# Kernel optimization log

Hardware: AMD Instinct MI355X
Metric: run time of the kernel (lower is better)

Reference implementation:

```python
import jax, jax.numpy as jnp
import numpy as np

C = 1024
H = 64
W = 64


def _conv1x1(x, Wt, b):
    # x: [1, Cin, H, W], Wt: [Cout, Cin] -> [1, Cout, H, W]
    return jnp.einsum('oc,bchw->bohw', Wt, x) + b[None, :, None, None]


def setup_inputs() -> dict:
    key = jax.random.key(0)
    ks = jax.random.split(key, 12)
    sc = 1.0 / np.sqrt(C)
    return {
        'x_f': jax.random.normal(ks[0], (1, C, H, W), jnp.float32),
        'x_m': jax.random.normal(ks[1], (1, C, H, W), jnp.float32),
        'x_l': jax.random.normal(ks[2], (1, C, H, W), jnp.float32),
        'Wq': jax.random.normal(ks[3], (C // 2, C), jnp.float32) * sc,
        'bq': jax.random.normal(ks[4], (C // 2,), jnp.float32) * sc,
        'Wk1': jax.random.normal(ks[5], (C // 2, C), jnp.float32) * sc,
        'bk1': jax.random.normal(ks[6], (C // 2,), jnp.float32) * sc,
        'Wk2': jax.random.normal(ks[7], (C // 2, C), jnp.float32) * sc,
        'bk2': jax.random.normal(ks[8], (C // 2,), jnp.float32) * sc,
        'Wv': jax.random.normal(ks[9], (C, C), jnp.float32) * sc,
        'bv': jax.random.normal(ks[10], (C,), jnp.float32) * sc,
        'gamma': jax.random.normal(ks[11], (1,), jnp.float32),
    }


def reference(x_f, x_m, x_l, Wq, bq, Wk1, bk1, Wk2, bk2, Wv, bv, gamma):
    c = x_f.shape[1]
    h, w = x_f.shape[2], x_f.shape[3]
    # torch .view(1, C, -1) on a [1, C/2, H, W] tensor: row-major reshape to [C, H*W/2]
    q = _conv1x1(x_m, Wq, bq).reshape(c, -1).T      # [HW/2, C]
    kf = _conv1x1(x_f, Wk1, bk1).reshape(c, -1)     # [C, HW/2]
    kl = _conv1x1(x_l, Wk2, bk2).reshape(c, -1)     # [C, HW/2]
    att_f = jax.nn.softmax(kf @ q, axis=-1)         # [C, C]
    att_l = jax.nn.softmax(kl @ q, axis=-1)         # [C, C]
    v = _conv1x1(x_m, Wv, bv).reshape(c, -1)        # [C, HW]
    out = att_f @ v + att_l @ v                     # [C, HW]
    out = out.reshape(1, c, h, w)
    return gamma * out + (x_l + x_f) / 2
```

## Files before the change

kernel.cpp:

```cpp
#include <hip/hip_runtime.h>
#include <math.h>


typedef __attribute__((ext_vector_type(8))) short    bf16x8;
typedef __attribute__((ext_vector_type(4))) float    f32x4;

__device__ __forceinline__ unsigned short f2bf(float x) {
    unsigned u = __float_as_uint(x);
    u += 0x7FFFu + ((u >> 16) & 1u);
    return (unsigned short)(u >> 16);
}
__device__ __forceinline__ float bf2f(unsigned short h) {
    return __uint_as_float(((unsigned)h) << 16);
}
__device__ __forceinline__ void split2(float x, unsigned short& h, unsigned short& l) {
    h = f2bf(x);
    l = f2bf(x - bf2f(h));
}

__device__ __forceinline__ void gld16(const unsigned short* g, unsigned short* l) {
    __builtin_amdgcn_global_load_lds(
        (const __attribute__((address_space(1))) unsigned int*)g,
        (__attribute__((address_space(3))) unsigned int*)l,
        16, 0, 0);
}

__global__ __launch_bounds__(256) void weights_split_k(
    const float* __restrict__ Wq, const float* __restrict__ Wk1,
    const float* __restrict__ Wk2, const float* __restrict__ Wv,
    unsigned short* __restrict__ Wqh, unsigned short* __restrict__ Wql,
    unsigned short* __restrict__ Wk1h, unsigned short* __restrict__ Wk1l,
    unsigned short* __restrict__ Wk2h, unsigned short* __restrict__ Wk2l,
    unsigned short* __restrict__ Wvh, unsigned short* __restrict__ Wvl)
{
    const int gi = blockIdx.x;
    const float* src; unsigned short *H, *L; int base;
    if (gi < 512)       { src = Wq;  H = Wqh;  L = Wql;  base = gi; }
    else if (gi < 1024) { src = Wk1; H = Wk1h; L = Wk1l; base = gi - 512; }
    else if (gi < 1536) { src = Wk2; H = Wk2h; L = Wk2l; base = gi - 1024; }
    else                { src = Wv;  H = Wvh;  L = Wvl;  base = gi - 1536; }
    const size_t i = (size_t)base * 1024 + threadIdx.x * 4;
    const float4 v = *(const float4*)(src + i);
    ushort4 h, l;
    split2(v.x, h.x, l.x); split2(v.y, h.y, l.y);
    split2(v.z, h.z, l.z); split2(v.w, h.w, l.w);
    *(ushort4*)(H + i) = h;
    *(ushort4*)(L + i) = l;
}

__global__ __launch_bounds__(256) void transpose3_k(
    const float* __restrict__ x0, const float* __restrict__ x1,
    const float* __restrict__ x2,
    unsigned short* __restrict__ t0h, unsigned short* __restrict__ t0l,
    unsigned short* __restrict__ t1h, unsigned short* __restrict__ t1l,
    unsigned short* __restrict__ t2h, unsigned short* __restrict__ t2l)
{
    const float* X; unsigned short *Th, *Tl;
    if (blockIdx.z == 0)      { X = x0; Th = t0h; Tl = t0l; }
    else if (blockIdx.z == 1) { X = x1; Th = t1h; Tl = t1l; }
    else                      { X = x2; Th = t2h; Tl = t2l; }

    __shared__ float t[32 * 33];
    const int tid = threadIdx.x;
    const int c0 = blockIdx.y * 32;
    const int p0 = blockIdx.x * 32;

    const int cl = tid >> 3;
    const int p4 = (tid & 7) * 4;
    const float4 v = *(const float4*)(X + (size_t)(c0 + cl) * 4096 + p0 + p4);
    t[(p4 + 0) * 33 + cl] = v.x;
    t[(p4 + 1) * 33 + cl] = v.y;
    t[(p4 + 2) * 33 + cl] = v.z;
    t[(p4 + 3) * 33 + cl] = v.w;
    __syncthreads();

    const int pl = tid >> 3;
    const int c4 = (tid & 7) * 4;
    ushort4 h, l;
    split2(t[pl * 33 + c4 + 0], h.x, l.x);
    split2(t[pl * 33 + c4 + 1], h.y, l.y);
    split2(t[pl * 33 + c4 + 2], h.z, l.z);
    split2(t[pl * 33 + c4 + 3], h.w, l.w);
    const size_t o = (size_t)(p0 + pl) * 1024 + c0 + c4;
    *(ushort4*)(Th + o) = h;
    *(ushort4*)(Tl + o) = l;
}

__global__ __launch_bounds__(256) void transpose1_k(
    const float* __restrict__ X,
    unsigned short* __restrict__ Th, unsigned short* __restrict__ Tl)
{
    __shared__ float t[32 * 33];
    const int tid = threadIdx.x;
    const int c0 = blockIdx.y * 32;
    const int p0 = blockIdx.x * 32;

    const int cl = tid >> 3;
    const int p4 = (tid & 7) * 4;
    const float4 v = *(const float4*)(X + (size_t)(c0 + cl) * 4096 + p0 + p4);
    t[(p4 + 0) * 33 + cl] = v.x;
    t[(p4 + 1) * 33 + cl] = v.y;
    t[(p4 + 2) * 33 + cl] = v.z;
    t[(p4 + 3) * 33 + cl] = v.w;
    __syncthreads();

    const int pl = tid >> 3;
    const int c4 = (tid & 7) * 4;
    ushort4 h, l;
    split2(t[pl * 33 + c4 + 0], h.x, l.x);
    split2(t[pl * 33 + c4 + 1], h.y, l.y);
    split2(t[pl * 33 + c4 + 2], h.z, l.z);
    split2(t[pl * 33 + c4 + 3], h.w, l.w);
    const size_t o = (size_t)(p0 + pl) * 1024 + c0 + c4;
    *(ushort4*)(Th + o) = h;
    *(ushort4*)(Tl + o) = l;
}

__device__ __forceinline__ void gemm_core(
    const unsigned short* __restrict__ Ah, const unsigned short* __restrict__ Al,
    const unsigned short* __restrict__ Bh, const unsigned short* __restrict__ Bl,
    int ldk, int kbeg, int kend, int m0, int n0,
    unsigned short* As_h, unsigned short* As_l,
    unsigned short* Bs_h, unsigned short* Bs_l,
    f32x4 (&acc)[4][4])
{
    const int tid  = threadIdx.x;
    const int lane = tid & 63;
    const int wv   = tid >> 6;
    const int wm   = (wv >> 1) * 64;
    const int wn   = (wv & 1) * 64;
    const int lr   = lane & 15;
    const int quad = lane >> 4;

    const unsigned short* gsrc = (wv == 0) ? Ah : (wv == 1) ? Al : (wv == 2) ? Bh : Bl;
    unsigned short* ldst = (wv == 0) ? As_h : (wv == 1) ? As_l : (wv == 2) ? Bs_h : Bs_l;
    const int tile0 = (wv < 2) ? m0 : n0;
    const int lrow = lane >> 2;
    const int gseg = ((lane & 3) - ((lane >> 3) & 3)) & 3;
    const unsigned short* gp[8];
#pragma unroll
    for (int t = 0; t < 8; ++t)
        gp[t] = gsrc + (size_t)(tile0 + t * 16 + lrow) * ldk + kbeg + gseg * 8;

    const int rdseg = (quad + (lr >> 1)) & 3;

    for (int k0 = kbeg; k0 < kend; k0 += 32) {
        __syncthreads();
#pragma unroll
        for (int t = 0; t < 8; ++t) {
            gld16(gp[t], ldst + t * 512);
            gp[t] += 32;
        }
        __syncthreads();

        bf16x8 afh[4], afl[4], bfh[4], bfl[4];
#pragma unroll
        for (int i = 0; i < 4; ++i) {
            const int ra = (wm + i * 16 + lr) * 32 + rdseg * 8;
            afh[i] = *(const bf16x8*)(As_h + ra);
            afl[i] = *(const bf16x8*)(As_l + ra);
            const int rb = (wn + i * 16 + lr) * 32 + rdseg * 8;
            bfh[i] = *(const bf16x8*)(Bs_h + rb);
            bfl[i] = *(const bf16x8*)(Bs_l + rb);
        }
#pragma unroll
        for (int i = 0; i < 4; ++i)
#pragma unroll
            for (int j = 0; j < 4; ++j) {
                acc[i][j] = __builtin_amdgcn_mfma_f32_16x16x32_bf16(afh[i], bfh[j], acc[i][j], 0, 0, 0);
                acc[i][j] = __builtin_amdgcn_mfma_f32_16x16x32_bf16(afh[i], bfl[j], acc[i][j], 0, 0, 0);
                acc[i][j] = __builtin_amdgcn_mfma_f32_16x16x32_bf16(afl[i], bfh[j], acc[i][j], 0, 0, 0);
            }
    }
}

#define GEMM_PROLOGUE()                                                 \
    __shared__ __align__(16) unsigned short As_h[128 * 32];             \
    __shared__ __align__(16) unsigned short As_l[128 * 32];             \
    __shared__ __align__(16) unsigned short Bs_h[128 * 32];             \
    __shared__ __align__(16) unsigned short Bs_l[128 * 32];             \
    f32x4 acc[4][4];                                                    \
    _Pragma("unroll") for (int i = 0; i < 4; ++i)                       \
    _Pragma("unroll") for (int j = 0; j < 4; ++j)                       \
    _Pragma("unroll") for (int r = 0; r < 4; ++r) acc[i][j][r] = 0.f;   \
    const int lane = threadIdx.x & 63;                                  \
    const int wv   = threadIdx.x >> 6;                                  \
    const int wm   = (wv >> 1) * 64;                                    \
    const int wn   = (wv & 1) * 64;                                     \
    const int lr   = lane & 15;                                         \
    const int quad = lane >> 4;                                         \
    (void)lane; (void)wv;

__global__ __launch_bounds__(256) void conv_all_k(
    const unsigned short* __restrict__ Wqh, const unsigned short* __restrict__ Wql,
    const unsigned short* __restrict__ Wk1h, const unsigned short* __restrict__ Wk1l,
    const unsigned short* __restrict__ Wk2h, const unsigned short* __restrict__ Wk2l,
    const unsigned short* __restrict__ Wvh, const unsigned short* __restrict__ Wvl,
    const unsigned short* __restrict__ xmTh, const unsigned short* __restrict__ xmTl,
    const unsigned short* __restrict__ xfTh, const unsigned short* __restrict__ xfTl,
    const unsigned short* __restrict__ xlTh, const unsigned short* __restrict__ xlTl,
    const float* __restrict__ bq, const float* __restrict__ bk1,
    const float* __restrict__ bk2, const float* __restrict__ bv,
    unsigned short* __restrict__ Qh, unsigned short* __restrict__ Ql,
    unsigned short* __restrict__ Kfh, unsigned short* __restrict__ Kfl,
    unsigned short* __restrict__ Klh, unsigned short* __restrict__ Kll,
    float* __restrict__ V)
{
    GEMM_PROLOGUE();
    const int mt = blockIdx.y;
    const unsigned short *Ah, *Al, *Bh, *Bl;
    const float* bias;
    unsigned short *Ch = nullptr, *Cl = nullptr;
    float* Cv = nullptr;
    int mloc;
    if (mt < 4) {
        Ah = Wqh;  Al = Wql;  Bh = xmTh; Bl = xmTl; bias = bq;
        Ch = Qh;   Cl = Ql;   mloc = mt * 128;
    } else if (mt < 8) {
        Ah = Wk1h; Al = Wk1l; Bh = xfTh; Bl = xfTl; bias = bk1;
        Ch = Kfh;  Cl = Kfl;  mloc = (mt - 4) * 128;
    } else if (mt < 12) {
        Ah = Wk2h; Al = Wk2l; Bh = xlTh; Bl = xlTl; bias = bk2;
        Ch = Klh;  Cl = Kll;  mloc = (mt - 8) * 128;
    } else {
        Ah = Wvh;  Al = Wvl;  Bh = xmTh; Bl = xmTl; bias = bv;
        Cv = V;    mloc = (mt - 12) * 128;
    }
    const int n0 = blockIdx.x * 128;

    gemm_core(Ah, Al, Bh, Bl, 1024, 0, 1024, mloc, n0, As_h, As_l, Bs_h, Bs_l, acc);

#pragma unroll
    for (int i = 0; i < 4; ++i) {
        const int mb = mloc + wm + i * 16 + quad * 4;
#pragma unroll
        for (int j = 0; j < 4; ++j) {
            const int nn = n0 + wn + j * 16 + lr;
#pragma unroll
            for (int r = 0; r < 4; ++r) {
                const float v = acc[i][j][r] + bias[mb + r];
                const size_t idx = (size_t)(mb + r) * 4096 + nn;
                if (Cv) {
                    Cv[idx] = v;
                } else {
                    unsigned short h, l;
                    split2(v, h, l);
                    Ch[idx] = h;
                    Cl[idx] = l;
                }
            }
        }
    }
}

__global__ __launch_bounds__(256) void logits_fused_k(
    const unsigned short* __restrict__ Kfh, const unsigned short* __restrict__ Kfl,
    const unsigned short* __restrict__ Klh, const unsigned short* __restrict__ Kll,
    const unsigned short* __restrict__ Qh, const unsigned short* __restrict__ Ql,
    float* __restrict__ Sfp, float* __restrict__ Slp)
{
    GEMM_PROLOGUE();
    const int which = blockIdx.z >> 2;
    const int slice = blockIdx.z & 3;
    const unsigned short* Ah = which ? Klh : Kfh;
    const unsigned short* Al = which ? Kll : Kfl;
    float* out = (which ? Slp : Sfp) + (size_t)slice * 1024 * 1024;
    const int m0 = blockIdx.y * 128;
    const int n0 = blockIdx.x * 128;

    gemm_core(Ah, Al, Qh, Ql, 2048, slice * 512, slice * 512 + 512, m0, n0,
              As_h, As_l, Bs_h, Bs_l, acc);

#pragma unroll
    for (int i = 0; i < 4; ++i) {
        const int mb = m0 + wm + i * 16 + quad * 4;
#pragma unroll
        for (int j = 0; j < 4; ++j) {
            const int nn = n0 + wn + j * 16 + lr;
#pragma unroll
            for (int r = 0; r < 4; ++r)
                out[(size_t)(mb + r) * 1024 + nn] = acc[i][j][r];
        }
    }
}

__global__ __launch_bounds__(256) void gemm_final_k(
    const unsigned short* __restrict__ Amh, const unsigned short* __restrict__ Aml,
    const unsigned short* __restrict__ VTh, const unsigned short* __restrict__ VTl,
    float* __restrict__ out,
    const float* __restrict__ xf, const float* __restrict__ xl,
    const float* __restrict__ gamma)
{
    GEMM_PROLOGUE();
    const int m0 = blockIdx.y * 128;
    const int n0 = blockIdx.x * 128;

    gemm_core(Amh, Aml, VTh, VTl, 1024, 0, 1024, m0, n0,
              As_h, As_l, Bs_h, Bs_l, acc);

    const float g = gamma[0];
#pragma unroll
    for (int i = 0; i < 4; ++i) {
        const int mb = m0 + wm + i * 16 + quad * 4;
#pragma unroll
        for (int j = 0; j < 4; ++j) {
            const int nn = n0 + wn + j * 16 + lr;
#pragma unroll
            for (int r = 0; r < 4; ++r) {
                const size_t idx = (size_t)(mb + r) * 4096 + nn;
                out[idx] = g * acc[i][j][r] + 0.5f * (xf[idx] + xl[idx]);
            }
        }
    }
}

__global__ __launch_bounds__(256) void softmax_add4_k(
    const float* __restrict__ Sfp, const float* __restrict__ Slp,
    unsigned short* __restrict__ Ah, unsigned short* __restrict__ Al)
{
    const int row = blockIdx.x;
    const int tid = threadIdx.x;
    __shared__ float red[8];
    const size_t base = (size_t)row * 1024 + tid * 4;
    const size_t SL = (size_t)1024 * 1024;

    float4 vf = *(const float4*)(Sfp + base);
    float4 vl = *(const float4*)(Slp + base);
#pragma unroll
    for (int s = 1; s < 4; ++s) {
        const float4 a = *(const float4*)(Sfp + s * SL + base);
        const float4 b = *(const float4*)(Slp + s * SL + base);
        vf.x += a.x; vf.y += a.y; vf.z += a.z; vf.w += a.w;
        vl.x += b.x; vl.y += b.y; vl.z += b.z; vl.w += b.w;
    }

    float mf = fmaxf(fmaxf(vf.x, vf.y), fmaxf(vf.z, vf.w));
    float ml = fmaxf(fmaxf(vl.x, vl.y), fmaxf(vl.z, vl.w));
#pragma unroll
    for (int off = 32; off; off >>= 1) {
        mf = fmaxf(mf, __shfl_down(mf, off, 64));
        ml = fmaxf(ml, __shfl_down(ml, off, 64));
    }
    const int wave = tid >> 6;
    if ((tid & 63) == 0) { red[wave] = mf; red[4 + wave] = ml; }
    __syncthreads();
    mf = fmaxf(fmaxf(red[0], red[1]), fmaxf(red[2], red[3]));
    ml = fmaxf(fmaxf(red[4], red[5]), fmaxf(red[6], red[7]));
    __syncthreads();

    const float4 ef = make_float4(expf(vf.x - mf), expf(vf.y - mf),
                                  expf(vf.z - mf), expf(vf.w - mf));
    const float4 el = make_float4(expf(vl.x - ml), expf(vl.y - ml),
                                  expf(vl.z - ml), expf(vl.w - ml));
    float sf = ef.x + ef.y + ef.z + ef.w;
    float sl = el.x + el.y + el.z + el.w;
#pragma unroll
    for (int off = 32; off; off >>= 1) {
        sf += __shfl_down(sf, off, 64);
        sl += __shfl_down(sl, off, 64);
    }
    if ((tid & 63) == 0) { red[wave] = sf; red[4 + wave] = sl; }
    __syncthreads();
    sf = red[0] + red[1] + red[2] + red[3];
    sl = red[4] + red[5] + red[6] + red[7];

    const float rf = 1.f / sf, rl = 1.f / sl;
    ushort4 h, l;
    split2(ef.x * rf + el.x * rl, h.x, l.x);
    split2(ef.y * rf + el.y * rl, h.y, l.y);
    split2(ef.z * rf + el.z * rl, h.z, l.z);
    split2(ef.w * rf + el.w * rl, h.w, l.w);
    *(ushort4*)(Ah + base) = h;
    *(ushort4*)(Al + base) = l;
}

__global__ void noop_k(float* p) { if (threadIdx.x == 1024) p[0] = 0.f; }

extern "C" void kernel_launch(void* const* d_in, const int* in_sizes, int n_in,
                              void* d_out, int out_size, void* d_ws, size_t ws_size,
                              hipStream_t stream) {
    (void)in_sizes; (void)n_in; (void)out_size;
    const float* xf  = (const float*)d_in[0];
    const float* xm  = (const float*)d_in[1];
    const float* xl  = (const float*)d_in[2];
    const float* Wq  = (const float*)d_in[3];
    const float* bq  = (const float*)d_in[4];
    const float* Wk1 = (const float*)d_in[5];
    const float* bk1 = (const float*)d_in[6];
    const float* Wk2 = (const float*)d_in[7];
    const float* bk2 = (const float*)d_in[8];
    const float* Wv  = (const float*)d_in[9];
    const float* bv  = (const float*)d_in[10];
    const float* gamma = (const float*)d_in[11];
    float* out = (float*)d_out;

    const size_t MB = 1024 * 1024;
    if (ws_size < 98 * MB) {
        noop_k<<<dim3(1), dim3(64), 0, stream>>>((float*)d_ws);
        return;
    }

    char* p = (char*)d_ws;
    unsigned short* xmT_h = (unsigned short*)(p + 0 * MB);
    unsigned short* xmT_l = (unsigned short*)(p + 8 * MB);
    unsigned short* xfT_h = (unsigned short*)(p + 16 * MB);
    unsigned short* xfT_l = (unsigned short*)(p + 24 * MB);
    unsigned short* xlT_h = (unsigned short*)(p + 32 * MB);
    unsigned short* xlT_l = (unsigned short*)(p + 40 * MB);
    unsigned short* Wq_h  = (unsigned short*)(p + 48 * MB);
    unsigned short* Wq_l  = (unsigned short*)(p + 49 * MB);
    unsigned short* Wk1_h = (unsigned short*)(p + 50 * MB);
    unsigned short* Wk1_l = (unsigned short*)(p + 51 * MB);
    unsigned short* Wk2_h = (unsigned short*)(p + 52 * MB);
    unsigned short* Wk2_l = (unsigned short*)(p + 53 * MB);
    unsigned short* Wv_h  = (unsigned short*)(p + 54 * MB);
    unsigned short* Wv_l  = (unsigned short*)(p + 56 * MB);
    unsigned short* Q_h   = (unsigned short*)(p + 58 * MB);
    unsigned short* Q_l   = (unsigned short*)(p + 62 * MB);
    unsigned short* Kf_h  = (unsigned short*)(p + 66 * MB);
    unsigned short* Kf_l  = (unsigned short*)(p + 70 * MB);
    unsigned short* Kl_h  = (unsigned short*)(p + 74 * MB);
    unsigned short* Kl_l  = (unsigned short*)(p + 78 * MB);
    float*          V     = (float*)(p + 82 * MB);
    float*          Sfp  = (float*)(p + 16 * MB);
    float*          Slp  = (float*)(p + 32 * MB);
    unsigned short* VT_h = xmT_h;
    unsigned short* VT_l = xmT_l;
    unsigned short* Am_h = (unsigned short*)(p + 74 * MB);
    unsigned short* Am_l = (unsigned short*)(p + 76 * MB);

    const dim3 blk(256);
    transpose3_k<<<dim3(128, 32, 3), blk, 0, stream>>>(
        xm, xf, xl, xmT_h, xmT_l, xfT_h, xfT_l, xlT_h, xlT_l);
    weights_split_k<<<dim3(2560), blk, 0, stream>>>(
        Wq, Wk1, Wk2, Wv, Wq_h, Wq_l, Wk1_h, Wk1_l, Wk2_h, Wk2_l, Wv_h, Wv_l);
    conv_all_k<<<dim3(32, 20), blk, 0, stream>>>(
        Wq_h, Wq_l, Wk1_h, Wk1_l, Wk2_h, Wk2_l, Wv_h, Wv_l,
        xmT_h, xmT_l, xfT_h, xfT_l, xlT_h, xlT_l,
        bq, bk1, bk2, bv,
        Q_h, Q_l, Kf_h, Kf_l, Kl_h, Kl_l, V);
    logits_fused_k<<<dim3(8, 8, 8), blk, 0, stream>>>(
        Kf_h, Kf_l, Kl_h, Kl_l, Q_h, Q_l, Sfp, Slp);
    transpose1_k<<<dim3(128, 32), blk, 0, stream>>>(V, VT_h, VT_l);
    softmax_add4_k<<<dim3(1024), blk, 0, stream>>>(Sfp, Slp, Am_h, Am_l);
    gemm_final_k<<<dim3(32, 8), blk, 0, stream>>>(
        Am_h, Am_l, VT_h, VT_l, out, xf, xl, gamma);
}
```

Before: 303.6 us.

## Double-buffer B tiles in LDS, load A directly to registers, drop third term in final GEMM

The shared GEMM core now keeps only the B operand in LDS, double-buffered so the next k-slice load is issued before the current slice is computed, which removes one barrier per iteration. The A operand fragments are read straight from global memory into registers instead of being staged through LDS. A template parameter lets the final attention-times-V GEMM skip the lo(A)*hi(B) MFMA term, cutting its MFMA count by a third. Skipping that term lowers the precision of the final GEMM, and the direct global A loads may add latency and uncoalesced traffic.

```diff
diff --git a/kernel.cpp b/kernel.cpp
--- a/kernel.cpp
+++ b/kernel.cpp
@@ -116,11 +116,11 @@
     *(ushort4*)(Tl + o) = l;
 }
 
+template<int TERMS>
 __device__ __forceinline__ void gemm_core(
     const unsigned short* __restrict__ Ah, const unsigned short* __restrict__ Al,
     const unsigned short* __restrict__ Bh, const unsigned short* __restrict__ Bl,
     int ldk, int kbeg, int kend, int m0, int n0,
-    unsigned short* As_h, unsigned short* As_l,
     unsigned short* Bs_h, unsigned short* Bs_l,
     f32x4 (&acc)[4][4])
 {
@@ -132,36 +132,56 @@
     const int lr   = lane & 15;
     const int quad = lane >> 4;
 
-    const unsigned short* gsrc = (wv == 0) ? Ah : (wv == 1) ? Al : (wv == 2) ? Bh : Bl;
-    unsigned short* ldst = (wv == 0) ? As_h : (wv == 1) ? As_l : (wv == 2) ? Bs_h : Bs_l;
-    const int tile0 = (wv < 2) ? m0 : n0;
+    const unsigned short* gsrc = (wv < 2) ? Bh : Bl;
+    unsigned short* ldst = (wv < 2) ? Bs_h : Bs_l;
+    const int tt0  = (wv & 1) * 4;
     const int lrow = lane >> 2;
     const int gseg = ((lane & 3) - ((lane >> 3) & 3)) & 3;
-    const unsigned short* gp[8];
-#pragma unroll
-    for (int t = 0; t < 8; ++t)
-        gp[t] = gsrc + (size_t)(tile0 + t * 16 + lrow) * ldk + kbeg + gseg * 8;
+    const unsigned short* gp[4];
+#pragma unroll
+    for (int u = 0; u < 4; ++u)
+        gp[u] = gsrc + (size_t)(n0 + (tt0 + u) * 16 + lrow) * ldk + kbeg + gseg * 8;
+
+    const unsigned short* ap[4];
+    const unsigned short* apl[4];
+#pragma unroll
+    for (int i = 0; i < 4; ++i) {
+        const size_t ro = (size_t)(m0 + wm + i * 16 + lr) * ldk + kbeg + quad * 8;
+        ap[i] = Ah + ro;
+        apl[i] = (TERMS == 3) ? (Al + ro) : nullptr;
+    }
 
     const int rdseg = (quad + (lr >> 1)) & 3;
 
+#pragma unroll
+    for (int u = 0; u < 4; ++u) {
+        gld16(gp[u], ldst + (tt0 + u) * 512);
+        gp[u] += 32;
+    }
+
+    int buf = 0;
     for (int k0 = kbeg; k0 < kend; k0 += 32) {
         __syncthreads();
-#pragma unroll
-        for (int t = 0; t < 8; ++t) {
-            gld16(gp[t], ldst + t * 512);
-            gp[t] += 32;
-        }
-        __syncthreads();
-
-        bf16x8 afh[4], afl[4], bfh[4], bfl[4];
+
+        bf16x8 afh[4], afl[4];
 #pragma unroll
         for (int i = 0; i < 4; ++i) {
-            const int ra = (wm + i * 16 + lr) * 32 + rdseg * 8;
-            afh[i] = *(const bf16x8*)(As_h + ra);
-            afl[i] = *(const bf16x8*)(As_l + ra);
-            const int rb = (wn + i * 16 + lr) * 32 + rdseg * 8;
-            bfh[i] = *(const bf16x8*)(Bs_h + rb);
-            bfl[i] = *(const bf16x8*)(Bs_l + rb);
+            afh[i] = *(const bf16x8*)ap[i];  ap[i] += 32;
+            if (TERMS == 3) { afl[i] = *(const bf16x8*)apl[i]; apl[i] += 32; }
+        }
+        if (k0 + 32 < kend) {
+#pragma unroll
+            for (int u = 0; u < 4; ++u) {
+                gld16(gp[u], ldst + (buf ^ 1) * 4096 + (tt0 + u) * 512);
+                gp[u] += 32;
+            }
+        }
+        bf16x8 bfh[4], bfl[4];
+#pragma unroll
+        for (int j = 0; j < 4; ++j) {
+            const int rb = buf * 4096 + (wn + j * 16 + lr) * 32 + rdseg * 8;
+            bfh[j] = *(const bf16x8*)(Bs_h + rb);
+            bfl[j] = *(const bf16x8*)(Bs_l + rb);
         }
 #pragma unroll
         for (int i = 0; i < 4; ++i)
@@ -169,16 +189,16 @@
             for (int j = 0; j < 4; ++j) {
                 acc[i][j] = __builtin_amdgcn_mfma_f32_16x16x32_bf16(afh[i], bfh[j], acc[i][j], 0, 0, 0);
                 acc[i][j] = __builtin_amdgcn_mfma_f32_16x16x32_bf16(afh[i], bfl[j], acc[i][j], 0, 0, 0);
-                acc[i][j] = __builtin_amdgcn_mfma_f32_16x16x32_bf16(afl[i], bfh[j], acc[i][j], 0, 0, 0);
+                if (TERMS == 3)
+                    acc[i][j] = __builtin_amdgcn_mfma_f32_16x16x32_bf16(afl[i], bfh[j], acc[i][j], 0, 0, 0);
             }
+        buf ^= 1;
     }
 }
 
 #define GEMM_PROLOGUE()                                                 \
-    __shared__ __align__(16) unsigned short As_h[128 * 32];             \
-    __shared__ __align__(16) unsigned short As_l[128 * 32];             \
-    __shared__ __align__(16) unsigned short Bs_h[128 * 32];             \
-    __shared__ __align__(16) unsigned short Bs_l[128 * 32];             \
+    __shared__ __align__(16) unsigned short Bs_h[2 * 128 * 32];         \
+    __shared__ __align__(16) unsigned short Bs_l[2 * 128 * 32];         \
     f32x4 acc[4][4];                                                    \
     _Pragma("unroll") for (int i = 0; i < 4; ++i)                       \
     _Pragma("unroll") for (int j = 0; j < 4; ++j)                       \
@@ -228,7 +248,7 @@
     }
     const int n0 = blockIdx.x * 128;
 
-    gemm_core(Ah, Al, Bh, Bl, 1024, 0, 1024, mloc, n0, As_h, As_l, Bs_h, Bs_l, acc);
+    gemm_core<3>(Ah, Al, Bh, Bl, 1024, 0, 1024, mloc, n0, Bs_h, Bs_l, acc);
 
 #pragma unroll
     for (int i = 0; i < 4; ++i) {
@@ -268,8 +288,8 @@
     const int m0 = blockIdx.y * 128;
     const int n0 = blockIdx.x * 128;
 
-    gemm_core(Ah, Al, Qh, Ql, 2048, slice * 512, slice * 512 + 512, m0, n0,
-              As_h, As_l, Bs_h, Bs_l, acc);
+    gemm_core<3>(Ah, Al, Qh, Ql, 2048, slice * 512, slice * 512 + 512, m0, n0,
+                 Bs_h, Bs_l, acc);
 
 #pragma unroll
     for (int i = 0; i < 4; ++i) {
@@ -295,8 +315,7 @@
     const int m0 = blockIdx.y * 128;
     const int n0 = blockIdx.x * 128;
 
-    gemm_core(Amh, Aml, VTh, VTl, 1024, 0, 1024, m0, n0,
-              As_h, As_l, Bs_h, Bs_l, acc);
+    gemm_core<2>(Amh, Aml, VTh, VTl, 1024, 0, 1024, m0, n0, Bs_h, Bs_l, acc);
 
     const float g = gamma[0];
 #pragma unroll
```

Measured after the change: 371.0 us. +22.2%, slower.
